# Performance work log

Hardware: AMD Instinct MI355X
Metric: run time of the kernel (lower is better)

## Reference

```python
import jax, jax.numpy as jnp
import numpy as np

B, T, D = 4, 4096, 1024

def setup_inputs() -> dict:
    key = jax.random.key(0)
    ks = jax.random.split(key, 7)
    s1 = 1.0 / np.sqrt(D)
    s2 = 1.0 / np.sqrt(2 * D)
    return {
        "x": jax.random.normal(ks[0], (B, T, D), jnp.float32),
        "W1": jax.random.uniform(ks[1], (D, 2 * D), jnp.float32, -s1, s1),      # Linear(D,2D,bias=False)
        "W2": jax.random.uniform(ks[2], (2 * D, 2 * D), jnp.float32, -s2, s2),  # Linear(2D,2D)
        "b2": jax.random.uniform(ks[3], (2 * D,), jnp.float32, -s2, s2),
        "conv_w": jax.random.uniform(ks[4], (D, 1, 3), jnp.float32, -1/np.sqrt(3), 1/np.sqrt(3)),  # depthwise k=3
        "gamma": jnp.ones((D,), jnp.float32),
        "beta": jnp.zeros((D,), jnp.float32),
    }

def _gated_scan(theta, alpha):
    # parallel stable scan: h_t = a_t * h_{t-1} + (1 - a_t) * tanh(theta_t), h_0 = 0
    a = jax.nn.sigmoid(alpha)
    b = (1.0 - a) * jnp.tanh(theta)
    def combine(c1, c2):
        a1, b1 = c1
        a2, b2 = c2
        return a1 * a2, a2 * b1 + b2
    _, h = jax.lax.associative_scan(combine, (a, b), axis=1)
    return h

def reference(x, W1, W2, b2, conv_w, gamma, beta):
    # morphism generator: Linear -> SiLU -> Linear
    mp = jax.nn.silu(x @ W1) @ W2 + b2                      # (B,T,2D)
    theta, alpha = jnp.split(mp, 2, axis=-1)
    semantic = _gated_scan(theta, alpha)                    # (B,T,D)
    # causal depthwise conv: left-pad 2, kernel 3, groups=D
    sc = jnp.transpose(semantic, (0, 2, 1))                 # (B,D,T)
    cb = jax.lax.conv_general_dilated(
        sc, conv_w, window_strides=(1,), padding=[(2, 0)],
        dimension_numbers=("NCH", "OIH", "NCH"), feature_group_count=D)
    cb = jax.nn.silu(jnp.transpose(cb, (0, 2, 1)))          # (B,T,D)
    y = semantic + 0.1 * cb
    # LayerNorm over D
    mu = jnp.mean(y, axis=-1, keepdims=True)
    var = jnp.mean(jnp.square(y - mu), axis=-1, keepdims=True)
    y = (y - mu) * jax.lax.rsqrt(var + 1e-5) * gamma + beta
    # dropout is identity in eval mode; L2 normalize (torch eps=1e-12)
    nrm = jnp.sqrt(jnp.sum(jnp.square(y), axis=-1, keepdims=True))
    return y / jnp.maximum(nrm, 1e-12)
```

## Files before the change

kernel.cpp:

```cpp
#include <hip/hip_runtime.h>
#include <cstdint>
#include <cstddef>

typedef __attribute__((ext_vector_type(8))) short bf16x8;
typedef __attribute__((ext_vector_type(4))) float f32x4;
typedef unsigned short u16;
typedef unsigned int u32;

__device__ __forceinline__ u16 f2bf(float f) {
  u32 u = __float_as_uint(f);
  u32 r = (u + 0x7fffu + ((u >> 16) & 1u)) >> 16;
  return (u16)r;
}
__device__ __forceinline__ float bf2f(u16 h) {
  return __uint_as_float(((u32)h) << 16);
}
__device__ __forceinline__ float fsilu(float v) { return v / (1.f + __expf(-v)); }
__device__ __forceinline__ float fsigmoid(float v) { return 1.f / (1.f + __expf(-v)); }

__device__ __forceinline__ void glds16(const void* g, void* l) {
  __builtin_amdgcn_global_load_lds(
      (const __attribute__((address_space(1))) void*)g,
      (__attribute__((address_space(3))) void*)l, 16, 0, 0);
}

#define FENCE_MEM() asm volatile("" ::: "memory")
#define BAR() __builtin_amdgcn_s_barrier()
#define VMCNT(n) asm volatile("s_waitcnt vmcnt(" #n ")" ::: "memory")
#define LGKMW(n)                                        \
  do {                                                  \
    asm volatile("s_waitcnt lgkmcnt(" #n ")" ::: "memory"); \
    __builtin_amdgcn_sched_barrier(0);                  \
  } while (0)


__global__ __launch_bounds__(256) void cast_bf16_vec(const float* __restrict__ src,
                                                     u16* __restrict__ dst, int n4) {
  int i = blockIdx.x * 256 + threadIdx.x;
  if (i >= n4) return;
  const float4 v = ((const float4*)src)[i];
  ushort4 o;
  o.x = f2bf(v.x); o.y = f2bf(v.y); o.z = f2bf(v.z); o.w = f2bf(v.w);
  ((ushort4*)dst)[i] = o;
}

__global__ void transpose_cast(const float* __restrict__ src, u16* __restrict__ dst,
                               int R, int C) {
  __shared__ float tile[32][33];
  int bx = blockIdx.x * 32;
  int by = blockIdx.y * 32;
  int tx = threadIdx.x, ty = threadIdx.y;
#pragma unroll
  for (int i = 0; i < 4; ++i)
    tile[ty + i * 8][tx] = src[(size_t)(by + ty + i * 8) * C + bx + tx];
  __syncthreads();
#pragma unroll
  for (int i = 0; i < 4; ++i)
    dst[(size_t)(bx + ty + i * 8) * R + by + tx] = f2bf(tile[tx][ty + i * 8]);
}


template <int EPI>
__global__ __launch_bounds__(512, 2) void gemm256(const u16* __restrict__ A,
                                                  const u16* __restrict__ Bt,
                                                  u16* __restrict__ Co,
                                                  const float* __restrict__ bias,
                                                  int M, int N, int K) {
  __shared__ char lds[131072];
  const int tid = threadIdx.x;
  const int lane = tid & 63;
  const int wid = tid >> 6;
  const int wr = wid >> 2;
  const int wc = wid & 3;

  const int gx = gridDim.x;
  const int nwg = gx * gridDim.y;
  const int bid = blockIdx.y * gx + blockIdx.x;
  const int swz = (bid & 7) * (nwg >> 3) + (bid >> 3);
  const long bm = (long)(swz / gx) * 256;
  const long bn = (long)(swz % gx) * 256;

  const int NT = K >> 6;

  const int r0 = tid >> 3, c0p = tid & 7;
  const int r1 = r0 + 64;
  const int gA0 = (r0 & 63) + ((r0 >> 6) << 7);
  const int gA1 = (r1 & 63) + ((r1 >> 6) << 7);
  const int gB0 = (r0 & 31) + ((r0 >> 5) << 6);
  const int gB1 = (r1 & 31) + ((r1 >> 5) << 6);
  const int cA0 = c0p ^ (r0 & 7);
  const size_t srcA0 = (size_t)(bm + gA0) * K + cA0 * 8;
  const size_t srcA1 = (size_t)(bm + gA1) * K + cA0 * 8;
  const size_t srcB0 = (size_t)(bn + gB0) * K + cA0 * 8;
  const size_t srcB1 = (size_t)(bn + gB1) * K + cA0 * 8;
  const int dstA0 = gA0 * 128 + c0p * 16;
  const int dstA1 = gA1 * 128 + c0p * 16;
  const int dstB0 = 32768 + gB0 * 128 + c0p * 16;
  const int dstB1 = 32768 + gB1 * 128 + c0p * 16;
  const size_t halfA = (size_t)64 * K;
  const size_t halfB = (size_t)32 * K;

#define STAGE_P(buf, t, pair)                                                        \
  do {                                                                               \
    if ((pair) == 0) {                                                               \
      glds16(A + srcA0 + (size_t)(t) * 64, lds + (buf) * 65536 + dstA0);             \
      glds16(A + srcA1 + (size_t)(t) * 64, lds + (buf) * 65536 + dstA1);             \
    } else if ((pair) == 1) {                                                        \
      glds16(A + srcA0 + halfA + (size_t)(t) * 64,                                   \
             lds + (buf) * 65536 + dstA0 + 8192);                                    \
      glds16(A + srcA1 + halfA + (size_t)(t) * 64,                                   \
             lds + (buf) * 65536 + dstA1 + 8192);                                    \
    } else if ((pair) == 2) {                                                        \
      glds16(Bt + srcB0 + (size_t)(t) * 64, lds + (buf) * 65536 + dstB0);            \
      glds16(Bt + srcB1 + (size_t)(t) * 64, lds + (buf) * 65536 + dstB1);            \
    } else {                                                                         \
      glds16(Bt + srcB0 + halfB + (size_t)(t) * 64,                                  \
             lds + (buf) * 65536 + dstB0 + 4096);                                    \
      glds16(Bt + srcB1 + halfB + (size_t)(t) * 64,                                  \
             lds + (buf) * 65536 + dstB1 + 4096);                                    \
    }                                                                                \
  } while (0)

  const int l15 = lane & 15, l3 = lane & 7, g4 = lane >> 4;
  const int aoff0 = (wr * 128 + l15) * 128 + ((g4 ^ l3) * 16);
  const int aoff1 = (wr * 128 + l15) * 128 + (((4 + g4) ^ l3) * 16);
  const int boff0 = 32768 + (wc * 64 + l15) * 128 + ((g4 ^ l3) * 16);
  const int boff1 = 32768 + (wc * 64 + l15) * 128 + (((4 + g4) ^ l3) * 16);

  f32x4 acc[8][4] = {};

#define READ_A(dst, q)                                                               \
  do {                                                                               \
    dst[0][0] = *(const bf16x8*)(base + aoff0 + ((q) * 2 + 0) * 2048);               \
    dst[0][1] = *(const bf16x8*)(base + aoff1 + ((q) * 2 + 0) * 2048);               \
    dst[1][0] = *(const bf16x8*)(base + aoff0 + ((q) * 2 + 1) * 2048);               \
    dst[1][1] = *(const bf16x8*)(base + aoff1 + ((q) * 2 + 1) * 2048);               \
  } while (0)

#define MFMA_Q(q, af)                                                                \
  do {                                                                               \
    __builtin_amdgcn_s_setprio(1);                                                   \
    _Pragma("unroll") for (int kh = 0; kh < 2; ++kh)                                 \
        _Pragma("unroll") for (int mm = 0; mm < 2; ++mm)                             \
            _Pragma("unroll") for (int nn = 0; nn < 4; ++nn) {                       \
      acc[(q) * 2 + mm][nn] = __builtin_amdgcn_mfma_f32_16x16x32_bf16(               \
          af[mm][kh], bfr[nn][kh], acc[(q) * 2 + mm][nn], 0, 0, 0);                  \
    }                                                                                \
    __builtin_amdgcn_s_setprio(0);                                                   \
  } while (0)

  STAGE_P(0, 0, 0);
  STAGE_P(0, 0, 1);
  STAGE_P(0, 0, 2);
  STAGE_P(0, 0, 3);
  VMCNT(0);
  FENCE_MEM();
  BAR();
  FENCE_MEM();

  for (int t = 0; t < NT; ++t) {
    const int p = t & 1;
    const char* base = lds + p * 65536;
    const bool s1 = (t + 1) < NT;

    bf16x8 bfr[4][2];
    bf16x8 afx[2][2], afy[2][2];

#pragma unroll
    for (int nn = 0; nn < 4; ++nn) {
      bfr[nn][0] = *(const bf16x8*)(base + boff0 + nn * 2048);
      bfr[nn][1] = *(const bf16x8*)(base + boff1 + nn * 2048);
    }
    READ_A(afx, 0);
    READ_A(afy, 1);
    if (s1) STAGE_P(p ^ 1, t + 1, 0);
    FENCE_MEM();
    LGKMW(4);
    MFMA_Q(0, afx);
    READ_A(afx, 2);
    if (s1) STAGE_P(p ^ 1, t + 1, 1);
    FENCE_MEM();
    LGKMW(4);
    MFMA_Q(1, afy);
    READ_A(afy, 3);
    if (s1) STAGE_P(p ^ 1, t + 1, 2);
    FENCE_MEM();
    LGKMW(4);
    MFMA_Q(2, afx);
    if (s1) STAGE_P(p ^ 1, t + 1, 3);
    FENCE_MEM();
    LGKMW(0);
    MFMA_Q(3, afy);

    VMCNT(0);
    FENCE_MEM();
    BAR();
    FENCE_MEM();
  }

  const int erow = (lane >> 4) * 4;
  const int ecol = lane & 15;
#pragma unroll
  for (int mf = 0; mf < 8; ++mf) {
#pragma unroll
    for (int nf = 0; nf < 4; ++nf) {
      const long col = bn + wc * 64 + nf * 16 + ecol;
      float badd = (EPI == 1) ? bias[col] : 0.f;
#pragma unroll
      for (int j = 0; j < 4; ++j) {
        const long row = bm + wr * 128 + mf * 16 + erow + j;
        float v = acc[mf][nf][j];
        if (EPI == 0) {
          v = fsilu(v);
        } else {
          v += badd;
          v = (col < 1024) ? tanhf(v) : fsigmoid(v);
        }
        Co[row * (long)N + col] = f2bf(v);
      }
    }
  }
#undef STAGE_P
#undef READ_A
#undef MFMA_Q
}


__global__ __launch_bounds__(256) void scan_stage1(const u16* __restrict__ sa,
                                                   float* __restrict__ cA,
                                                   float* __restrict__ cB) {
  const int tid = blockIdx.x * 256 + threadIdx.x;
  const int d = tid & 1023;
  const int chunk = (tid >> 10) & 63;
  const int b = tid >> 16;
  const size_t base = ((size_t)(b * 4096 + chunk * 64)) * 2048 + d;
  float Ac = 1.f, Bc = 0.f;
#pragma unroll 4
  for (int t = 0; t < 64; ++t) {
    float s = bf2f(sa[base + (size_t)t * 2048]);
    float a = bf2f(sa[base + (size_t)t * 2048 + 1024]);
    Bc = a * Bc + (1.f - a) * s;
    Ac *= a;
  }
  cA[tid] = Ac;
  cB[tid] = Bc;
}

__global__ __launch_bounds__(256) void scan_stage2(const float* __restrict__ cA,
                                                   const float* __restrict__ cB,
                                                   float* __restrict__ hstart) {
  const int tid = blockIdx.x * 256 + threadIdx.x;
  const int d = tid & 1023;
  const int b = tid >> 10;
  float h = 0.f;
  for (int c = 0; c < 64; ++c) {
    const size_t i = ((size_t)(b * 64 + c)) * 1024 + d;
    hstart[i] = h;
    h = cA[i] * h + cB[i];
  }
}

__global__ __launch_bounds__(256) void scan_stage3(const u16* __restrict__ sa,
                                                   const float* __restrict__ hstart,
                                                   float* __restrict__ sem) {
  const int tid = blockIdx.x * 256 + threadIdx.x;
  const int d = tid & 1023;
  const int chunk = (tid >> 10) & 63;
  const int b = tid >> 16;
  const size_t m0 = (size_t)(b * 4096 + chunk * 64);
  const size_t base = m0 * 2048 + d;
  float h = hstart[tid];
#pragma unroll 4
  for (int t = 0; t < 64; ++t) {
    float s = bf2f(sa[base + (size_t)t * 2048]);
    float a = bf2f(sa[base + (size_t)t * 2048 + 1024]);
    h = a * h + (1.f - a) * s;
    sem[(m0 + t) * 1024 + d] = h;
  }
}


__global__ __launch_bounds__(256) void finalize(const float* __restrict__ sem,
                                                const float* __restrict__ cw,
                                                const float* __restrict__ gamma,
                                                const float* __restrict__ beta,
                                                float* __restrict__ out) {
  const int r = blockIdx.x;
  const int t = r & 4095;
  const int tid = threadIdx.x;
  const int lane = tid & 63, wid = tid >> 6;
  const int d0 = tid * 4;
  const float4 zero = make_float4(0.f, 0.f, 0.f, 0.f);
  float4 s0 = ((const float4*)(sem + (size_t)r * 1024))[tid];
  float4 s1 = (t >= 1) ? ((const float4*)(sem + (size_t)(r - 1) * 1024))[tid] : zero;
  float4 s2 = (t >= 2) ? ((const float4*)(sem + (size_t)(r - 2) * 1024))[tid] : zero;
  float a0[4] = {s0.x, s0.y, s0.z, s0.w};
  float a1[4] = {s1.x, s1.y, s1.z, s1.w};
  float a2[4] = {s2.x, s2.y, s2.z, s2.w};
  float y[4];
  float vs = 0.f, vq = 0.f;
#pragma unroll
  for (int j = 0; j < 4; ++j) {
    int d = d0 + j;
    float cb = cw[d * 3] * a2[j] + cw[d * 3 + 1] * a1[j] + cw[d * 3 + 2] * a0[j];
    cb = fsilu(cb);
    y[j] = a0[j] + 0.1f * cb;
    vs += y[j];
    vq += y[j] * y[j];
  }
  __shared__ float rb[2][4];
#pragma unroll
  for (int o = 32; o > 0; o >>= 1) {
    vs += __shfl_down(vs, o);
    vq += __shfl_down(vq, o);
  }
  if (lane == 0) { rb[0][wid] = vs; rb[1][wid] = vq; }
  __syncthreads();
  float tsum = rb[0][0] + rb[0][1] + rb[0][2] + rb[0][3];
  float tss = rb[1][0] + rb[1][1] + rb[1][2] + rb[1][3];
  float mu = tsum * (1.f / 1024.f);
  float var = tss * (1.f / 1024.f) - mu * mu;
  float rstd = rsqrtf(var + 1e-5f);
  float yn[4];
  float q = 0.f;
#pragma unroll
  for (int j = 0; j < 4; ++j) {
    int d = d0 + j;
    yn[j] = (y[j] - mu) * rstd * gamma[d] + beta[d];
    q += yn[j] * yn[j];
  }
#pragma unroll
  for (int o = 32; o > 0; o >>= 1) q += __shfl_down(q, o);
  __syncthreads();
  if (lane == 0) rb[0][wid] = q;
  __syncthreads();
  float nrm = sqrtf(rb[0][0] + rb[0][1] + rb[0][2] + rb[0][3]);
  float scale = 1.f / fmaxf(nrm, 1e-12f);
  float4 o4 = make_float4(yn[0] * scale, yn[1] * scale, yn[2] * scale, yn[3] * scale);
  ((float4*)(out + (size_t)r * 1024))[tid] = o4;
}


extern "C" void kernel_launch(void* const* d_in, const int* in_sizes, int n_in,
                              void* d_out, int out_size, void* d_ws, size_t ws_size,
                              hipStream_t stream) {
  const float* x = (const float*)d_in[0];
  const float* W1 = (const float*)d_in[1];
  const float* W2 = (const float*)d_in[2];
  const float* b2 = (const float*)d_in[3];
  const float* cw = (const float*)d_in[4];
  const float* gamma = (const float*)d_in[5];
  const float* beta = (const float*)d_in[6];
  float* out = (float*)d_out;
  char* ws = (char*)d_ws;

  u16* xb = (u16*)(ws);
  u16* w1t = (u16*)(ws + 33554432);
  u16* w2t = (u16*)(ws + 37748736);
  u16* h1 = (u16*)(ws + 46137344);
  float* sem = (float*)(ws + 46137344);
  u16* sa = (u16*)(ws + 113246208);
  float* cA = (float*)(ws);
  float* cB = (float*)(ws + 1048576);
  float* hstart = (float*)(ws + 2097152);

  cast_bf16_vec<<<16384, 256, 0, stream>>>(x, xb, 4194304);
  transpose_cast<<<dim3(64, 32), dim3(32, 8), 0, stream>>>(W1, w1t, 1024, 2048);
  transpose_cast<<<dim3(64, 64), dim3(32, 8), 0, stream>>>(W2, w2t, 2048, 2048);
  gemm256<0><<<dim3(8, 64), 512, 0, stream>>>(xb, w1t, h1, nullptr, 16384, 2048, 1024);
  gemm256<1><<<dim3(8, 64), 512, 0, stream>>>(h1, w2t, sa, b2, 16384, 2048, 2048);
  scan_stage1<<<1024, 256, 0, stream>>>(sa, cA, cB);
  scan_stage2<<<16, 256, 0, stream>>>(cA, cB, hstart);
  scan_stage3<<<1024, 256, 0, stream>>>(sa, hstart, sem);
  finalize<<<16384, 256, 0, stream>>>(sem, cw, gamma, beta, out);
}
```

Measured before the change: 334.5 us.

## Restructure GEMM main loop into k-half phases with barrier-separated staged prefetch

Reorganizes the bf16 MFMA GEMM inner loop so each K-tile is processed in four phases split by k-half and m-half, reading B fragments per k-half instead of all at once. The staged global-to-LDS loads for the next tile are reordered (B first) and waited on with partial vmcnt counts instead of a full drain at the end of the iteration. The aim is to cut register pressure and overlap more of the global loads with MFMA work. In exchange it adds several workgroup barriers per iteration and full lgkmcnt(0) waits, which may serialize the waves more.

```diff
diff --git a/kernel.cpp b/kernel.cpp
--- a/kernel.cpp
+++ b/kernel.cpp
@@ -27,10 +27,10 @@
 #define FENCE_MEM() asm volatile("" ::: "memory")
 #define BAR() __builtin_amdgcn_s_barrier()
 #define VMCNT(n) asm volatile("s_waitcnt vmcnt(" #n ")" ::: "memory")
-#define LGKMW(n)                                        \
-  do {                                                  \
-    asm volatile("s_waitcnt lgkmcnt(" #n ")" ::: "memory"); \
-    __builtin_amdgcn_sched_barrier(0);                  \
+#define LGKM0()                                             \
+  do {                                                      \
+    asm volatile("s_waitcnt lgkmcnt(0)" ::: "memory");      \
+    __builtin_amdgcn_sched_barrier(0);                      \
   } while (0)
 
 
@@ -122,38 +122,43 @@
   } while (0)
 
   const int l15 = lane & 15, l3 = lane & 7, g4 = lane >> 4;
-  const int aoff0 = (wr * 128 + l15) * 128 + ((g4 ^ l3) * 16);
-  const int aoff1 = (wr * 128 + l15) * 128 + (((4 + g4) ^ l3) * 16);
-  const int boff0 = 32768 + (wc * 64 + l15) * 128 + ((g4 ^ l3) * 16);
-  const int boff1 = 32768 + (wc * 64 + l15) * 128 + (((4 + g4) ^ l3) * 16);
+  const int chnk0 = ((g4 ^ l3)) * 16;
+  const int chnk1 = (((4 + g4) ^ l3)) * 16;
+  const int arow = (wr * 128 + l15) * 128;
+  const int brow = 32768 + (wc * 64 + l15) * 128;
 
   f32x4 acc[8][4] = {};
 
-#define READ_A(dst, q)                                                               \
+#define RD_A(dst, mh, kh)                                                            \
   do {                                                                               \
-    dst[0][0] = *(const bf16x8*)(base + aoff0 + ((q) * 2 + 0) * 2048);               \
-    dst[0][1] = *(const bf16x8*)(base + aoff1 + ((q) * 2 + 0) * 2048);               \
-    dst[1][0] = *(const bf16x8*)(base + aoff0 + ((q) * 2 + 1) * 2048);               \
-    dst[1][1] = *(const bf16x8*)(base + aoff1 + ((q) * 2 + 1) * 2048);               \
-  } while (0)
-
-#define MFMA_Q(q, af)                                                                \
+    _Pragma("unroll") for (int mm = 0; mm < 4; ++mm)                                 \
+        dst[mm] = *(const bf16x8*)(base + arow + ((mh) * 4 + mm) * 2048 +            \
+                                   ((kh) ? chnk1 : chnk0));                          \
+  } while (0)
+
+#define RD_B(dst, kh)                                                                \
+  do {                                                                               \
+    _Pragma("unroll") for (int nn = 0; nn < 4; ++nn)                                 \
+        dst[nn] = *(const bf16x8*)(base + brow + nn * 2048 +                         \
+                                   ((kh) ? chnk1 : chnk0));                          \
+  } while (0)
+
+#define MF(mh, af, bk)                                                               \
   do {                                                                               \
     __builtin_amdgcn_s_setprio(1);                                                   \
-    _Pragma("unroll") for (int kh = 0; kh < 2; ++kh)                                 \
-        _Pragma("unroll") for (int mm = 0; mm < 2; ++mm)                             \
-            _Pragma("unroll") for (int nn = 0; nn < 4; ++nn) {                       \
-      acc[(q) * 2 + mm][nn] = __builtin_amdgcn_mfma_f32_16x16x32_bf16(               \
-          af[mm][kh], bfr[nn][kh], acc[(q) * 2 + mm][nn], 0, 0, 0);                  \
+    _Pragma("unroll") for (int mm = 0; mm < 4; ++mm)                                 \
+        _Pragma("unroll") for (int nn = 0; nn < 4; ++nn) {                           \
+      acc[(mh) * 4 + mm][nn] = __builtin_amdgcn_mfma_f32_16x16x32_bf16(              \
+          af[mm], bk[nn], acc[(mh) * 4 + mm][nn], 0, 0, 0);                          \
     }                                                                                \
     __builtin_amdgcn_s_setprio(0);                                                   \
   } while (0)
 
+  STAGE_P(0, 0, 2);
+  STAGE_P(0, 0, 3);
   STAGE_P(0, 0, 0);
   STAGE_P(0, 0, 1);
-  STAGE_P(0, 0, 2);
-  STAGE_P(0, 0, 3);
-  VMCNT(0);
+  VMCNT(2);
   FENCE_MEM();
   BAR();
   FENCE_MEM();
@@ -162,37 +167,54 @@
     const int p = t & 1;
     const char* base = lds + p * 65536;
     const bool s1 = (t + 1) < NT;
-
-    bf16x8 bfr[4][2];
-    bf16x8 afx[2][2], afy[2][2];
-
-#pragma unroll
-    for (int nn = 0; nn < 4; ++nn) {
-      bfr[nn][0] = *(const bf16x8*)(base + boff0 + nn * 2048);
-      bfr[nn][1] = *(const bf16x8*)(base + boff1 + nn * 2048);
+    bf16x8 a0[4], a1[4], bk0[4], bk1[4];
+
+    RD_B(bk0, 0);
+    RD_A(a0, 0, 0);
+    if (s1) STAGE_P(p ^ 1, t + 1, 2);
+    FENCE_MEM();
+    BAR();
+    LGKM0();
+    MF(0, a0, bk0);
+    FENCE_MEM();
+    BAR();
+    FENCE_MEM();
+
+    RD_B(bk1, 1);
+    RD_A(a1, 0, 1);
+    if (s1) {
+      STAGE_P(p ^ 1, t + 1, 3);
+      VMCNT(4);
+    } else {
+      VMCNT(0);
     }
-    READ_A(afx, 0);
-    READ_A(afy, 1);
+    FENCE_MEM();
+    BAR();
+    LGKM0();
+    MF(0, a1, bk1);
+    FENCE_MEM();
+    BAR();
+    FENCE_MEM();
+
+    RD_A(a0, 1, 0);
     if (s1) STAGE_P(p ^ 1, t + 1, 0);
     FENCE_MEM();
-    LGKMW(4);
-    MFMA_Q(0, afx);
-    READ_A(afx, 2);
-    if (s1) STAGE_P(p ^ 1, t + 1, 1);
-    FENCE_MEM();
-    LGKMW(4);
-    MFMA_Q(1, afy);
-    READ_A(afy, 3);
-    if (s1) STAGE_P(p ^ 1, t + 1, 2);
-    FENCE_MEM();
-    LGKMW(4);
-    MFMA_Q(2, afx);
-    if (s1) STAGE_P(p ^ 1, t + 1, 3);
-    FENCE_MEM();
-    LGKMW(0);
-    MFMA_Q(3, afy);
-
-    VMCNT(0);
+    BAR();
+    LGKM0();
+    MF(1, a0, bk0);
+    FENCE_MEM();
+    BAR();
+    FENCE_MEM();
+
+    RD_A(a1, 1, 1);
+    if (s1) {
+      STAGE_P(p ^ 1, t + 1, 1);
+      VMCNT(2);
+    }
+    FENCE_MEM();
+    BAR();
+    LGKM0();
+    MF(1, a1, bk1);
     FENCE_MEM();
     BAR();
     FENCE_MEM();
@@ -221,8 +243,9 @@
     }
   }
 #undef STAGE_P
-#undef READ_A
-#undef MFMA_Q
+#undef RD_A
+#undef RD_B
+#undef MF
 }
 
 
```

After: 341.9 us. 2.2% more time.

## Fuse scan pass three with conv, LayerNorm and L2 normalize; use fast tanh

Applied to the files above, without the earlier changes.

Replaces the separate scan_stage3 and finalize kernels with one kernel. Each block walks a 64-step chunk across the full D=1024 row, keeps the last two hidden states in registers for the causal depthwise conv, and computes LayerNorm and the L2 norm in a single reduction pass using algebraic sums of gamma and beta terms. Stage 1 now also saves the chunk prefix before the last step, so the first steps of each chunk can rebuild the two previous states from the prior chunk. This removes the fp32 semantic buffer round trip through HBM. In exchange the new kernel launches only 256 blocks and runs 64 sequential steps, each with a block-wide reduction and two barriers, prefetching only one step ahead. The GEMM epilogue also swaps tanhf for an exp-based tanh.

```diff
diff --git a/kernel.cpp b/kernel.cpp
--- a/kernel.cpp
+++ b/kernel.cpp
@@ -17,6 +17,9 @@
 }
 __device__ __forceinline__ float fsilu(float v) { return v / (1.f + __expf(-v)); }
 __device__ __forceinline__ float fsigmoid(float v) { return 1.f / (1.f + __expf(-v)); }
+__device__ __forceinline__ float ftanh(float v) {
+  return 1.f - 2.f / (__expf(2.f * v) + 1.f);
+}
 
 __device__ __forceinline__ void glds16(const void* g, void* l) {
   __builtin_amdgcn_global_load_lds(
@@ -214,7 +217,7 @@
           v = fsilu(v);
         } else {
           v += badd;
-          v = (col < 1024) ? tanhf(v) : fsigmoid(v);
+          v = (col < 1024) ? ftanh(v) : fsigmoid(v);
         }
         Co[row * (long)N + col] = f2bf(v);
       }
@@ -228,7 +231,9 @@
 
 __global__ __launch_bounds__(256) void scan_stage1(const u16* __restrict__ sa,
                                                    float* __restrict__ cA,
-                                                   float* __restrict__ cB) {
+                                                   float* __restrict__ cB,
+                                                   float* __restrict__ cA63,
+                                                   float* __restrict__ cB63) {
   const int tid = blockIdx.x * 256 + threadIdx.x;
   const int d = tid & 1023;
   const int chunk = (tid >> 10) & 63;
@@ -236,9 +241,17 @@
   const size_t base = ((size_t)(b * 4096 + chunk * 64)) * 2048 + d;
   float Ac = 1.f, Bc = 0.f;
 #pragma unroll 4
-  for (int t = 0; t < 64; ++t) {
+  for (int t = 0; t < 63; ++t) {
     float s = bf2f(sa[base + (size_t)t * 2048]);
     float a = bf2f(sa[base + (size_t)t * 2048 + 1024]);
+    Bc = a * Bc + (1.f - a) * s;
+    Ac *= a;
+  }
+  cA63[tid] = Ac;
+  cB63[tid] = Bc;
+  {
+    float s = bf2f(sa[base + (size_t)63 * 2048]);
+    float a = bf2f(sa[base + (size_t)63 * 2048 + 1024]);
     Bc = a * Bc + (1.f - a) * s;
     Ac *= a;
   }
@@ -260,84 +273,133 @@
   }
 }
 
-__global__ __launch_bounds__(256) void scan_stage3(const u16* __restrict__ sa,
-                                                   const float* __restrict__ hstart,
-                                                   float* __restrict__ sem) {
-  const int tid = blockIdx.x * 256 + threadIdx.x;
-  const int d = tid & 1023;
-  const int chunk = (tid >> 10) & 63;
-  const int b = tid >> 16;
-  const size_t m0 = (size_t)(b * 4096 + chunk * 64);
-  const size_t base = m0 * 2048 + d;
-  float h = hstart[tid];
-#pragma unroll 4
-  for (int t = 0; t < 64; ++t) {
-    float s = bf2f(sa[base + (size_t)t * 2048]);
-    float a = bf2f(sa[base + (size_t)t * 2048 + 1024]);
-    h = a * h + (1.f - a) * s;
-    sem[(m0 + t) * 1024 + d] = h;
-  }
-}
-
-
-__global__ __launch_bounds__(256) void finalize(const float* __restrict__ sem,
-                                                const float* __restrict__ cw,
-                                                const float* __restrict__ gamma,
-                                                const float* __restrict__ beta,
-                                                float* __restrict__ out) {
-  const int r = blockIdx.x;
-  const int t = r & 4095;
+__global__ __launch_bounds__(256) void scan3_fused(
+    const u16* __restrict__ sa, const float* __restrict__ hstart,
+    const float* __restrict__ cA63, const float* __restrict__ cB63,
+    const float* __restrict__ cw, const float* __restrict__ gamma,
+    const float* __restrict__ beta, float* __restrict__ out) {
+  const int blk = blockIdx.x;
+  const int c = blk & 63;
   const int tid = threadIdx.x;
   const int lane = tid & 63, wid = tid >> 6;
   const int d0 = tid * 4;
-  const float4 zero = make_float4(0.f, 0.f, 0.f, 0.f);
-  float4 s0 = ((const float4*)(sem + (size_t)r * 1024))[tid];
-  float4 s1 = (t >= 1) ? ((const float4*)(sem + (size_t)(r - 1) * 1024))[tid] : zero;
-  float4 s2 = (t >= 2) ? ((const float4*)(sem + (size_t)(r - 2) * 1024))[tid] : zero;
-  float a0[4] = {s0.x, s0.y, s0.z, s0.w};
-  float a1[4] = {s1.x, s1.y, s1.z, s1.w};
-  float a2[4] = {s2.x, s2.y, s2.z, s2.w};
-  float y[4];
-  float vs = 0.f, vq = 0.f;
+  const size_t m0 = (size_t)(blk >> 6) * 4096 + (size_t)c * 64;
+
+  __shared__ float red[4][8];
+
+  const float4 gv = *(const float4*)(gamma + d0);
+  const float4 bv = *(const float4*)(beta + d0);
+  const float g[4] = {gv.x, gv.y, gv.z, gv.w};
+  const float be[4] = {bv.x, bv.y, bv.z, bv.w};
+  float w0[4], w1[4], w2[4];
 #pragma unroll
   for (int j = 0; j < 4; ++j) {
-    int d = d0 + j;
-    float cb = cw[d * 3] * a2[j] + cw[d * 3 + 1] * a1[j] + cw[d * 3 + 2] * a0[j];
-    cb = fsilu(cb);
-    y[j] = a0[j] + 0.1f * cb;
-    vs += y[j];
-    vq += y[j] * y[j];
-  }
-  __shared__ float rb[2][4];
+    w0[j] = cw[(d0 + j) * 3];
+    w1[j] = cw[(d0 + j) * 3 + 1];
+    w2[j] = cw[(d0 + j) * 3 + 2];
+  }
+
+  const size_t hidx = (size_t)blk * 1024 + d0;
+  const float4 hs = *(const float4*)(hstart + hidx);
+  float h1v[4] = {hs.x, hs.y, hs.z, hs.w};
+  float h2v[4] = {0.f, 0.f, 0.f, 0.f};
+  if (c > 0) {
+    const float4 hp = *(const float4*)(hstart + hidx - 1024);
+    const float4 a63 = *(const float4*)(cA63 + hidx - 1024);
+    const float4 b63 = *(const float4*)(cB63 + hidx - 1024);
+    h2v[0] = a63.x * hp.x + b63.x;
+    h2v[1] = a63.y * hp.y + b63.y;
+    h2v[2] = a63.z * hp.z + b63.z;
+    h2v[3] = a63.w * hp.w + b63.w;
+  }
+
+  float sg2 = 0.f, sgb = 0.f, sb2 = 0.f;
+#pragma unroll
+  for (int j = 0; j < 4; ++j) {
+    sg2 += g[j] * g[j];
+    sgb += g[j] * be[j];
+    sb2 += be[j] * be[j];
+  }
 #pragma unroll
   for (int o = 32; o > 0; o >>= 1) {
-    vs += __shfl_down(vs, o);
-    vq += __shfl_down(vq, o);
-  }
-  if (lane == 0) { rb[0][wid] = vs; rb[1][wid] = vq; }
+    sg2 += __shfl_down(sg2, o);
+    sgb += __shfl_down(sgb, o);
+    sb2 += __shfl_down(sb2, o);
+  }
+  if (lane == 0) { red[wid][5] = sg2; red[wid][6] = sgb; red[wid][7] = sb2; }
   __syncthreads();
-  float tsum = rb[0][0] + rb[0][1] + rb[0][2] + rb[0][3];
-  float tss = rb[1][0] + rb[1][1] + rb[1][2] + rb[1][3];
-  float mu = tsum * (1.f / 1024.f);
-  float var = tss * (1.f / 1024.f) - mu * mu;
-  float rstd = rsqrtf(var + 1e-5f);
-  float yn[4];
-  float q = 0.f;
-#pragma unroll
-  for (int j = 0; j < 4; ++j) {
-    int d = d0 + j;
-    yn[j] = (y[j] - mu) * rstd * gamma[d] + beta[d];
-    q += yn[j] * yn[j];
-  }
-#pragma unroll
-  for (int o = 32; o > 0; o >>= 1) q += __shfl_down(q, o);
+  const float Sg2 = red[0][5] + red[1][5] + red[2][5] + red[3][5];
+  const float Sgb = red[0][6] + red[1][6] + red[2][6] + red[3][6];
+  const float Sb2 = red[0][7] + red[1][7] + red[2][7] + red[3][7];
   __syncthreads();
-  if (lane == 0) rb[0][wid] = q;
-  __syncthreads();
-  float nrm = sqrtf(rb[0][0] + rb[0][1] + rb[0][2] + rb[0][3]);
-  float scale = 1.f / fmaxf(nrm, 1e-12f);
-  float4 o4 = make_float4(yn[0] * scale, yn[1] * scale, yn[2] * scale, yn[3] * scale);
-  ((float4*)(out + (size_t)r * 1024))[tid] = o4;
+
+  const u16* ps = sa + m0 * 2048 + d0;
+  ushort4 sv = *(const ushort4*)(ps);
+  ushort4 av = *(const ushort4*)(ps + 1024);
+
+  for (int t = 0; t < 64; ++t) {
+    ushort4 svn, avn;
+    if (t + 1 < 64) {
+      svn = *(const ushort4*)(ps + (size_t)(t + 1) * 2048);
+      avn = *(const ushort4*)(ps + (size_t)(t + 1) * 2048 + 1024);
+    }
+    const float sarr[4] = {bf2f(sv.x), bf2f(sv.y), bf2f(sv.z), bf2f(sv.w)};
+    const float aarr[4] = {bf2f(av.x), bf2f(av.y), bf2f(av.z), bf2f(av.w)};
+    float y[4];
+    float s1 = 0.f, s2 = 0.f, g1 = 0.f, g2 = 0.f, gb = 0.f;
+#pragma unroll
+    for (int j = 0; j < 4; ++j) {
+      const float a = aarr[j];
+      const float h = a * h1v[j] + (1.f - a) * sarr[j];
+      float cb = w0[j] * h2v[j] + w1[j] * h1v[j] + w2[j] * h;
+      cb = fsilu(cb);
+      y[j] = h + 0.1f * cb;
+      h2v[j] = h1v[j];
+      h1v[j] = h;
+      s1 += y[j];
+      s2 += y[j] * y[j];
+      const float gy = g[j] * y[j];
+      g1 += g[j] * gy;
+      g2 += gy * gy;
+      gb += be[j] * gy;
+    }
+    float v0 = s1, v1 = s2, v2 = g1, v3 = g2, v4 = gb;
+#pragma unroll
+    for (int o = 32; o > 0; o >>= 1) {
+      v0 += __shfl_down(v0, o);
+      v1 += __shfl_down(v1, o);
+      v2 += __shfl_down(v2, o);
+      v3 += __shfl_down(v3, o);
+      v4 += __shfl_down(v4, o);
+    }
+    if (lane == 0) {
+      red[wid][0] = v0; red[wid][1] = v1; red[wid][2] = v2;
+      red[wid][3] = v3; red[wid][4] = v4;
+    }
+    __syncthreads();
+    const float S1 = red[0][0] + red[1][0] + red[2][0] + red[3][0];
+    const float S2 = red[0][1] + red[1][1] + red[2][1] + red[3][1];
+    const float G1 = red[0][2] + red[1][2] + red[2][2] + red[3][2];
+    const float G2 = red[0][3] + red[1][3] + red[2][3] + red[3][3];
+    const float GB = red[0][4] + red[1][4] + red[2][4] + red[3][4];
+    const float mu = S1 * (1.f / 1024.f);
+    const float var = S2 * (1.f / 1024.f) - mu * mu;
+    const float rstd = rsqrtf(var + 1e-5f);
+    const float sge2 = G2 - 2.f * mu * G1 + mu * mu * Sg2;
+    const float sgbe = GB - mu * Sgb;
+    const float nrm2 = rstd * rstd * sge2 + 2.f * rstd * sgbe + Sb2;
+    const float nrm = sqrtf(fmaxf(nrm2, 0.f));
+    const float scale = 1.f / fmaxf(nrm, 1e-12f);
+    float4 o4;
+    o4.x = (g[0] * (y[0] - mu) * rstd + be[0]) * scale;
+    o4.y = (g[1] * (y[1] - mu) * rstd + be[1]) * scale;
+    o4.z = (g[2] * (y[2] - mu) * rstd + be[2]) * scale;
+    o4.w = (g[3] * (y[3] - mu) * rstd + be[3]) * scale;
+    *(float4*)(out + (m0 + t) * 1024 + d0) = o4;
+    __syncthreads();
+    sv = svn;
+    av = avn;
+  }
 }
 
 
@@ -358,19 +420,19 @@
   u16* w1t = (u16*)(ws + 33554432);
   u16* w2t = (u16*)(ws + 37748736);
   u16* h1 = (u16*)(ws + 46137344);
-  float* sem = (float*)(ws + 46137344);
   u16* sa = (u16*)(ws + 113246208);
   float* cA = (float*)(ws);
   float* cB = (float*)(ws + 1048576);
   float* hstart = (float*)(ws + 2097152);
+  float* cA63 = (float*)(ws + 3145728);
+  float* cB63 = (float*)(ws + 4194304);
 
   cast_bf16_vec<<<16384, 256, 0, stream>>>(x, xb, 4194304);
   transpose_cast<<<dim3(64, 32), dim3(32, 8), 0, stream>>>(W1, w1t, 1024, 2048);
   transpose_cast<<<dim3(64, 64), dim3(32, 8), 0, stream>>>(W2, w2t, 2048, 2048);
   gemm256<0><<<dim3(8, 64), 512, 0, stream>>>(xb, w1t, h1, nullptr, 16384, 2048, 1024);
   gemm256<1><<<dim3(8, 64), 512, 0, stream>>>(h1, w2t, sa, b2, 16384, 2048, 2048);
-  scan_stage1<<<1024, 256, 0, stream>>>(sa, cA, cB);
+  scan_stage1<<<1024, 256, 0, stream>>>(sa, cA, cB, cA63, cB63);
   scan_stage2<<<16, 256, 0, stream>>>(cA, cB, hstart);
-  scan_stage3<<<1024, 256, 0, stream>>>(sa, hstart, sem);
-  finalize<<<16384, 256, 0, stream>>>(sem, cw, gamma, beta, out);
-}
+  scan3_fused<<<256, 256, 0, stream>>>(sa, hstart, cA63, cB63, cw, gamma, beta, out);
+}
```

After: 329.5 us, median of 2. About the same (-1.5%).
